# Kernel tuning notes

Measured on AMD Instinct MI355X. Metric: run time of the kernel, lower is better.

The kernel has to match this reference:

```python
import jax, jax.numpy as jnp
import numpy as np

B, T, I, H, L = 64, 2048, 128, 128, 2  # batch, seq_len, input, hidden, layers


def setup_inputs() -> dict:
    key = jax.random.key(0)
    ks = jax.random.split(key, 6)
    w = lambda k, shape: jax.random.normal(k, shape, dtype=jnp.float32) * 0.05
    return {
        "x": jax.random.normal(ks[0], (B, T, I), dtype=jnp.float32),
        "Wx0": w(ks[1], (4 * H, I)),
        "Wh0": w(ks[2], (4 * H, H)),
        "b0": jnp.zeros((4 * H,), jnp.float32),
        "Wx1": w(ks[3], (4 * H, H)),
        "Wh1": w(ks[4], (4 * H, H)),
        "b1": jnp.zeros((4 * H,), jnp.float32),
    }


def _cell(x_t, h, c, Wx, Wh, b):
    # fused-gate GEMM; gate order (i, f, g, o) matches the torch cell exactly
    gates = x_t @ Wx.T + h @ Wh.T + b  # [B, 4H]
    i, f, g, o = jnp.split(gates, 4, axis=-1)
    i = jax.nn.sigmoid(i)
    f = jax.nn.sigmoid(f)
    g = jnp.tanh(g)
    o = jax.nn.sigmoid(o)
    c_new = f * c + i * g
    h_new = o * jnp.tanh(c_new)
    return h_new, c_new


def reference(x, Wx0, Wh0, b0, Wx1, Wh1, b1):
    params = [(Wx0, Wh0, b0), (Wx1, Wh1, b1)]
    bsz = x.shape[0]
    hidden = Wh0.shape[1]
    h0 = jnp.zeros((L, bsz, hidden), x.dtype)
    c0 = jnp.zeros((L, bsz, hidden), x.dtype)

    def step(carry, x_t):
        h, c = carry
        hs, cs = [], []
        inp = x_t
        for l, (Wx, Wh, b) in enumerate(params):  # fixed, tiny layer loop
            hl, cl = _cell(inp, h[l], c[l], Wx, Wh, b)
            inp = hl
            hs.append(hl)
            cs.append(cl)
        return (jnp.stack(hs), jnp.stack(cs)), inp

    (hT, cT), ys = jax.lax.scan(step, (h0, c0), jnp.swapaxes(x, 0, 1))
    output = jnp.swapaxes(ys, 0, 1)  # [B, T, H], top-layer hidden states
    return output, hT, cT
```

## Files before the change

### kernel.cpp

```cpp
#include <hip/hip_runtime.h>
#include <hip/hip_fp16.h>

#define BB 64
#define TT 2048
#define II 128
#define HH 128
#define NG 512
#define CH 128
#define NCH (TT / CH)
#define DYN_LDS 81984

typedef _Float16 h2_t __attribute__((ext_vector_type(2)));

#if defined(__has_builtin)
#if __has_builtin(__builtin_amdgcn_fdot2)
#define HAVE_FDOT2 1
#endif
#endif

__device__ __forceinline__ float fdot2f(h2_t a, h2_t b, float c) {
#ifdef HAVE_FDOT2
  return __builtin_amdgcn_fdot2(a, b, c, false);
#else
  return c + (float)a[0] * (float)b[0] + (float)a[1] * (float)b[1];
#endif
}

__device__ __forceinline__ float fast_sigmoid(float x) {
  float t = __builtin_amdgcn_exp2f(-1.4426950408889634f * x);
  return __builtin_amdgcn_rcpf(1.0f + t);
}
__device__ __forceinline__ float act_gate(float x, bool tanh_sel) {
  float xx = tanh_sel ? 2.0f * x : x;
  float s = fast_sigmoid(xx);
  return tanh_sel ? 2.0f * s - 1.0f : s;
}
__device__ __forceinline__ float fast_tanh(float x) {
  return 2.0f * fast_sigmoid(2.0f * x) - 1.0f;
}

__device__ __forceinline__ float dpp_xor1(float x) {
  return __int_as_float(__builtin_amdgcn_update_dpp(0, __float_as_int(x), 0xB1, 0xF, 0xF, true));
}
__device__ __forceinline__ float dpp_xor2(float x) {
  return __int_as_float(__builtin_amdgcn_update_dpp(0, __float_as_int(x), 0x4E, 0xF, 0xF, true));
}

__device__ __forceinline__ void bar_lds() {
  __builtin_amdgcn_fence(__ATOMIC_RELEASE, "workgroup", "local");
  __builtin_amdgcn_s_barrier();
  __builtin_amdgcn_fence(__ATOMIC_ACQUIRE, "workgroup", "local");
}

union LD4 {
  float4 f4;
  h2_t h[4];
};
union LDB {
  uint4 u4;
  h2_t h[4];
};

__device__ __forceinline__ unsigned aload(unsigned* p) { return atomicAdd(p, 0u); }

__global__ void w_transpose2(const float* __restrict__ W0, float* __restrict__ T0,
                             const float* __restrict__ W1, float* __restrict__ T1) {
  int bid = blockIdx.x;
  const float* W = (bid < 256) ? W0 : W1;
  float* T = (bid < 256) ? T0 : T1;
  int idx = (bid & 255) * 256 + threadIdx.x;
  int n = idx >> 7;
  int k = idx & 127;
  T[k * NG + n] = W[idx];
}

__global__ __launch_bounds__(256) void xg_gemm_pro(const float* __restrict__ X,
                                                   const float* __restrict__ WT,
                                                   const float* __restrict__ bias,
                                                   __half* __restrict__ Xg) {
  __shared__ float As[64][132];
  __shared__ float Bs[128][64];
  const int bx = blockIdx.x;
  const size_t m0 = (size_t)(bx >> 2) * TT + (bx & 3) * 64;
  const int n0 = blockIdx.y * 64;
  const int tid = threadIdx.x;

  {
    const float4* xv = (const float4*)(X + m0 * II);
#pragma unroll
    for (int r = 0; r < 8; ++r) {
      int f = tid + 256 * r;
      int m = f >> 5;
      int c4 = f & 31;
      float4 v = xv[m * 32 + c4];
      *(float4*)&As[m][c4 * 4] = v;
    }
  }
  {
#pragma unroll
    for (int r = 0; r < 8; ++r) {
      int f = tid + 256 * r;
      int k = f >> 4;
      int q = f & 15;
      float4 v = *(const float4*)(WT + (size_t)k * NG + n0 + q * 4);
      *(float4*)&Bs[k][q * 4] = v;
    }
  }
  __syncthreads();

  const int tx = tid & 15;
  const int ty = tid >> 4;
  float acc[4][4];
#pragma unroll
  for (int i = 0; i < 4; ++i)
#pragma unroll
    for (int j = 0; j < 4; ++j) acc[i][j] = 0.0f;

#pragma unroll 4
  for (int k = 0; k < 128; ++k) {
    float a0 = As[ty * 4 + 0][k];
    float a1 = As[ty * 4 + 1][k];
    float a2 = As[ty * 4 + 2][k];
    float a3 = As[ty * 4 + 3][k];
    float4 bv = *(const float4*)&Bs[k][tx * 4];
    acc[0][0] = fmaf(a0, bv.x, acc[0][0]);
    acc[0][1] = fmaf(a0, bv.y, acc[0][1]);
    acc[0][2] = fmaf(a0, bv.z, acc[0][2]);
    acc[0][3] = fmaf(a0, bv.w, acc[0][3]);
    acc[1][0] = fmaf(a1, bv.x, acc[1][0]);
    acc[1][1] = fmaf(a1, bv.y, acc[1][1]);
    acc[1][2] = fmaf(a1, bv.z, acc[1][2]);
    acc[1][3] = fmaf(a1, bv.w, acc[1][3]);
    acc[2][0] = fmaf(a2, bv.x, acc[2][0]);
    acc[2][1] = fmaf(a2, bv.y, acc[2][1]);
    acc[2][2] = fmaf(a2, bv.z, acc[2][2]);
    acc[2][3] = fmaf(a2, bv.w, acc[2][3]);
    acc[3][0] = fmaf(a3, bv.x, acc[3][0]);
    acc[3][1] = fmaf(a3, bv.y, acc[3][1]);
    acc[3][2] = fmaf(a3, bv.z, acc[3][2]);
    acc[3][3] = fmaf(a3, bv.w, acc[3][3]);
  }

  float4 bvec = *(const float4*)(bias + n0 + tx * 4);
#pragma unroll
  for (int i = 0; i < 4; ++i) {
    size_t m = m0 + ty * 4 + i;
    __half2* dst = (__half2*)(Xg + m * NG + n0 + tx * 4);
    dst[0] = __halves2half2(__float2half(acc[i][0] + bvec.x),
                            __float2half(acc[i][1] + bvec.y));
    dst[1] = __halves2half2(__float2half(acc[i][2] + bvec.z),
                            __float2half(acc[i][3] + bvec.w));
  }
}


__device__ __forceinline__ void roleA(int b, int n, char* smem,
    const __half* Xg, const float* __restrict__ Wh0,
    float* __restrict__ out, __half* hstream,
    unsigned* flag0, unsigned* flagX)
{
  const int j = n >> 2;
  const int p = n & 3;
  const bool tsel = (p == 2);

  h2_t wh[4][16];
#pragma unroll
  for (int g = 0; g < 4; ++g) {
    const float2* ph = (const float2*)(Wh0 + (size_t)(g * 128 + j) * HH + p * 32);
#pragma unroll
    for (int k = 0; k < 16; ++k) {
      float2 v = ph[k];
      wh[g][k][0] = (_Float16)v.x;
      wh[g][k][1] = (_Float16)v.y;
    }
  }

  _Float16(*hb)[HH] = (_Float16(*)[HH])smem;
  if (n < HH) {
    hb[0][n] = (_Float16)0.0f;
    hb[1][n] = (_Float16)0.0f;
  }
  float c = 0.0f, hv = 0.0f;
  __syncthreads();

  const __half* xs = Xg + (size_t)b * TT * NG + p * 128 + j;
  float* hT = out + (size_t)BB * TT * HH;
  float* cT = hT + 2 * BB * HH;
  __half* hsp = hstream + (size_t)b * TT * HH + j;

#pragma unroll 1
  for (int cc = 0; cc < NCH; ++cc) {
    if (cc >= 2) {
      if (n == 0) {
        while (aload(flagX + b * NCH + cc) < 2u) __builtin_amdgcn_s_sleep(1);
      }
      __syncthreads();
      __builtin_amdgcn_fence(__ATOMIC_ACQUIRE, "agent");
    }
    __half xg_c = xs[(size_t)(cc * CH) * NG];

#pragma unroll 1
    for (int s = 0; s < CH; ++s) {
      const int i = cc * CH + s;
      __half xg_n = (s + 1 < CH) ? xs[(size_t)(i + 1) * NG] : __float2half(0.0f);

      const char* H = (const char*)hb[i & 1] + p * 64;
      float s0a = 0.f, s0b = 0.f, s1a = 0.f, s1b = 0.f;
      float s2a = 0.f, s2b = 0.f, s3a = 0.f, s3b = 0.f;
#pragma unroll
      for (int q = 0; q < 4; ++q) {
        LD4 u;
        u.f4 = *(const float4*)(H + q * 16);
        const int m = q * 4;
        s0a = fdot2f(wh[0][m + 0], u.h[0], s0a);
        s0b = fdot2f(wh[0][m + 2], u.h[2], s0b);
        s1a = fdot2f(wh[1][m + 0], u.h[0], s1a);
        s1b = fdot2f(wh[1][m + 2], u.h[2], s1b);
        s2a = fdot2f(wh[2][m + 0], u.h[0], s2a);
        s2b = fdot2f(wh[2][m + 2], u.h[2], s2b);
        s3a = fdot2f(wh[3][m + 0], u.h[0], s3a);
        s3b = fdot2f(wh[3][m + 2], u.h[2], s3b);
        s0a = fdot2f(wh[0][m + 1], u.h[1], s0a);
        s0b = fdot2f(wh[0][m + 3], u.h[3], s0b);
        s1a = fdot2f(wh[1][m + 1], u.h[1], s1a);
        s1b = fdot2f(wh[1][m + 3], u.h[3], s1b);
        s2a = fdot2f(wh[2][m + 1], u.h[1], s2a);
        s2b = fdot2f(wh[2][m + 3], u.h[3], s2b);
        s3a = fdot2f(wh[3][m + 1], u.h[1], s3a);
        s3b = fdot2f(wh[3][m + 3], u.h[3], s3b);
      }
      float a0 = s0a + s0b, a1 = s1a + s1b, a2 = s2a + s2b, a3 = s3a + s3b;

      float k01 = (p & 1) ? a1 : a0;
      float u01 = (p & 1) ? a0 : a1;
      float r01 = k01 + dpp_xor1(u01);
      float k23 = (p & 1) ? a3 : a2;
      float u23 = (p & 1) ? a2 : a3;
      float r23 = k23 + dpp_xor1(u23);
      float kA = (p & 2) ? r23 : r01;
      float uA = (p & 2) ? r01 : r23;
      float sL = kA + dpp_xor2(uA);
      float aL = act_gate(sL + __half2float(xg_c), tsel);
      float fg = dpp_xor1(aL);
      float gg = dpp_xor2(aL);
      float og = dpp_xor2(fg);
      if (p == 0) {
        c = fg * c + aL * gg;
        hv = og * fast_tanh(c);
        _Float16 hf = (_Float16)hv;
        hb[(i & 1) ^ 1][j] = hf;
        *(_Float16*)(hsp + (size_t)i * HH) = hf;
      }
      bar_lds();
      xg_c = xg_n;
    }
    __syncthreads();
    if (n == 0) {
      __builtin_amdgcn_fence(__ATOMIC_RELEASE, "agent");
      atomicExch(flag0 + b * NCH + cc, 1u);
    }
  }

  if (p == 0) {
    hT[b * HH + j] = hv;
    cT[b * HH + j] = c;
  }
}

__device__ __forceinline__ void roleC(int cidx, int n, char* smem,
    __half* Xg, const __half* hstream, const float* __restrict__ x,
    const float* __restrict__ WT0, const float* __restrict__ b0,
    const float* __restrict__ WT1, const float* __restrict__ b1,
    unsigned* flag0, unsigned* flagC, unsigned* flagX)
{
  const int b = cidx >> 1;
  const int half = cidx & 1;
  h2_t(*As2)[68] = (h2_t(*)[68])smem;
  h2_t(*Bs2)[64] = (h2_t(*)[64])(smem + 64 * 68 * 4);

  const int ty = n >> 4;
  const int tx = n & 15;
  const int mf = n >> 3;
  const int sf = n & 7;

#pragma unroll 1
  for (int cc = 0; cc < NCH; ++cc) {
    if (cc + 2 < NCH) {
      const int t0x = (cc + 2) * CH + half * 64;
      {
        const float4* sx = (const float4*)(x + ((size_t)b * TT + t0x + mf) * II + sf * 16);
        float4 p0 = sx[0], p1 = sx[1], p2 = sx[2], p3 = sx[3];
        h2_t r[8];
        r[0][0] = (_Float16)p0.x; r[0][1] = (_Float16)p0.y;
        r[1][0] = (_Float16)p0.z; r[1][1] = (_Float16)p0.w;
        r[2][0] = (_Float16)p1.x; r[2][1] = (_Float16)p1.y;
        r[3][0] = (_Float16)p1.z; r[3][1] = (_Float16)p1.w;
        r[4][0] = (_Float16)p2.x; r[4][1] = (_Float16)p2.y;
        r[5][0] = (_Float16)p2.z; r[5][1] = (_Float16)p2.w;
        r[6][0] = (_Float16)p3.x; r[6][1] = (_Float16)p3.y;
        r[7][0] = (_Float16)p3.z; r[7][1] = (_Float16)p3.w;
        *(uint4*)&As2[mf][sf * 8] = *(uint4*)&r[0];
        *(uint4*)&As2[mf][sf * 8 + 4] = *(uint4*)&r[4];
      }
#pragma unroll 1
      for (int nt = 0; nt < 8; ++nt) {
        __syncthreads();
        {
          const int kp = n >> 3, cg = n & 7;
          const float4* w0 = (const float4*)(WT0 + (size_t)(2 * kp) * NG + nt * 64 + cg * 8);
          const float4* w1 = (const float4*)(WT0 + (size_t)(2 * kp + 1) * NG + nt * 64 + cg * 8);
          float4 x0 = w0[0], x1 = w0[1];
          float4 y0 = w1[0], y1 = w1[1];
          h2_t r[8];
          r[0][0] = (_Float16)x0.x; r[0][1] = (_Float16)y0.x;
          r[1][0] = (_Float16)x0.y; r[1][1] = (_Float16)y0.y;
          r[2][0] = (_Float16)x0.z; r[2][1] = (_Float16)y0.z;
          r[3][0] = (_Float16)x0.w; r[3][1] = (_Float16)y0.w;
          r[4][0] = (_Float16)x1.x; r[4][1] = (_Float16)y1.x;
          r[5][0] = (_Float16)x1.y; r[5][1] = (_Float16)y1.y;
          r[6][0] = (_Float16)x1.z; r[6][1] = (_Float16)y1.z;
          r[7][0] = (_Float16)x1.w; r[7][1] = (_Float16)y1.w;
          *(uint4*)&Bs2[kp][cg * 8] = *(uint4*)&r[0];
          *(uint4*)&Bs2[kp][cg * 8 + 4] = *(uint4*)&r[4];
        }
        __syncthreads();

        float acc[2][4];
#pragma unroll
        for (int r = 0; r < 2; ++r)
#pragma unroll
          for (int q = 0; q < 4; ++q) acc[r][q] = 0.0f;
#pragma unroll 4
        for (int k4 = 0; k4 < 16; ++k4) {
          LDB ua0, ua1;
          ua0.u4 = *(const uint4*)&As2[ty * 2][k4 * 4];
          ua1.u4 = *(const uint4*)&As2[ty * 2 + 1][k4 * 4];
#pragma unroll
          for (int t = 0; t < 4; ++t) {
            LDB ub;
            ub.u4 = *(const uint4*)&Bs2[k4 * 4 + t][tx * 4];
            acc[0][0] = fdot2f(ua0.h[t], ub.h[0], acc[0][0]);
            acc[0][1] = fdot2f(ua0.h[t], ub.h[1], acc[0][1]);
            acc[0][2] = fdot2f(ua0.h[t], ub.h[2], acc[0][2]);
            acc[0][3] = fdot2f(ua0.h[t], ub.h[3], acc[0][3]);
            acc[1][0] = fdot2f(ua1.h[t], ub.h[0], acc[1][0]);
            acc[1][1] = fdot2f(ua1.h[t], ub.h[1], acc[1][1]);
            acc[1][2] = fdot2f(ua1.h[t], ub.h[2], acc[1][2]);
            acc[1][3] = fdot2f(ua1.h[t], ub.h[3], acc[1][3]);
          }
        }
        const int col = nt * 64 + tx * 4;
        float4 bv = *(const float4*)(b0 + col);
#pragma unroll
        for (int r = 0; r < 2; ++r) {
          __half2* d = (__half2*)(Xg + ((size_t)b * TT + t0x + ty * 2 + r) * NG + col);
          d[0] = __halves2half2(__float2half(acc[r][0] + bv.x),
                                __float2half(acc[r][1] + bv.y));
          d[1] = __halves2half2(__float2half(acc[r][2] + bv.z),
                                __float2half(acc[r][3] + bv.w));
        }
      }
      __syncthreads();
      if (n == 0) {
        __builtin_amdgcn_fence(__ATOMIC_RELEASE, "agent");
        atomicAdd(flagX + b * NCH + cc + 2, 1u);
      }
    }

    if (n == 0) {
      while (aload(flag0 + b * NCH + cc) < 1u) __builtin_amdgcn_s_sleep(8);
    }
    __syncthreads();
    __builtin_amdgcn_fence(__ATOMIC_ACQUIRE, "agent");

    const int t0 = cc * CH + half * 64;
    {
      const uint4* src = (const uint4*)(hstream + ((size_t)b * TT + t0 + mf) * HH + sf * 16);
      uint4 v0 = src[0], v1 = src[1];
      *(uint4*)&As2[mf][sf * 8] = v0;
      *(uint4*)&As2[mf][sf * 8 + 4] = v1;
    }
#pragma unroll 1
    for (int nt = 0; nt < 8; ++nt) {
      __syncthreads();
      {
        const int kp = n >> 3, cg = n & 7;
        const float4* w0 = (const float4*)(WT1 + (size_t)(2 * kp) * NG + nt * 64 + cg * 8);
        const float4* w1 = (const float4*)(WT1 + (size_t)(2 * kp + 1) * NG + nt * 64 + cg * 8);
        float4 x0 = w0[0], x1 = w0[1];
        float4 y0 = w1[0], y1 = w1[1];
        h2_t r[8];
        r[0][0] = (_Float16)x0.x; r[0][1] = (_Float16)y0.x;
        r[1][0] = (_Float16)x0.y; r[1][1] = (_Float16)y0.y;
        r[2][0] = (_Float16)x0.z; r[2][1] = (_Float16)y0.z;
        r[3][0] = (_Float16)x0.w; r[3][1] = (_Float16)y0.w;
        r[4][0] = (_Float16)x1.x; r[4][1] = (_Float16)y1.x;
        r[5][0] = (_Float16)x1.y; r[5][1] = (_Float16)y1.y;
        r[6][0] = (_Float16)x1.z; r[6][1] = (_Float16)y1.z;
        r[7][0] = (_Float16)x1.w; r[7][1] = (_Float16)y1.w;
        *(uint4*)&Bs2[kp][cg * 8] = *(uint4*)&r[0];
        *(uint4*)&Bs2[kp][cg * 8 + 4] = *(uint4*)&r[4];
      }
      __syncthreads();

      float acc[2][4];
#pragma unroll
      for (int r = 0; r < 2; ++r)
#pragma unroll
        for (int q = 0; q < 4; ++q) acc[r][q] = 0.0f;
#pragma unroll 4
      for (int k4 = 0; k4 < 16; ++k4) {
        LDB ua0, ua1;
        ua0.u4 = *(const uint4*)&As2[ty * 2][k4 * 4];
        ua1.u4 = *(const uint4*)&As2[ty * 2 + 1][k4 * 4];
#pragma unroll
        for (int t = 0; t < 4; ++t) {
          LDB ub;
          ub.u4 = *(const uint4*)&Bs2[k4 * 4 + t][tx * 4];
          acc[0][0] = fdot2f(ua0.h[t], ub.h[0], acc[0][0]);
          acc[0][1] = fdot2f(ua0.h[t], ub.h[1], acc[0][1]);
          acc[0][2] = fdot2f(ua0.h[t], ub.h[2], acc[0][2]);
          acc[0][3] = fdot2f(ua0.h[t], ub.h[3], acc[0][3]);
          acc[1][0] = fdot2f(ua1.h[t], ub.h[0], acc[1][0]);
          acc[1][1] = fdot2f(ua1.h[t], ub.h[1], acc[1][1]);
          acc[1][2] = fdot2f(ua1.h[t], ub.h[2], acc[1][2]);
          acc[1][3] = fdot2f(ua1.h[t], ub.h[3], acc[1][3]);
        }
      }
      const int col = nt * 64 + tx * 4;
      float4 bv = *(const float4*)(b1 + col);
#pragma unroll
      for (int r = 0; r < 2; ++r) {
        __half2* d = (__half2*)(Xg + ((size_t)b * TT + t0 + ty * 2 + r) * NG + col);
        d[0] = __halves2half2(__float2half(acc[r][0] + bv.x),
                              __float2half(acc[r][1] + bv.y));
        d[1] = __halves2half2(__float2half(acc[r][2] + bv.z),
                              __float2half(acc[r][3] + bv.w));
      }
    }
    __syncthreads();
    if (n == 0) {
      __builtin_amdgcn_fence(__ATOMIC_RELEASE, "agent");
      atomicAdd(flagC + b * NCH + cc, 1u);
    }
  }
}

__device__ __forceinline__ void roleB(int b, int n, char* smem,
    const __half* Xg, const float* __restrict__ Wh1,
    float* __restrict__ out, unsigned* flagC)
{
  const int j = n >> 2;
  const int p = n & 3;
  const bool tsel = (p == 2);

  h2_t wh[4][16];
#pragma unroll
  for (int g = 0; g < 4; ++g) {
    const float2* ph = (const float2*)(Wh1 + (size_t)(g * 128 + j) * HH + p * 32);
#pragma unroll
    for (int k = 0; k < 16; ++k) {
      float2 v = ph[k];
      wh[g][k][0] = (_Float16)v.x;
      wh[g][k][1] = (_Float16)v.y;
    }
  }

  _Float16(*hb)[HH] = (_Float16(*)[HH])smem;
  if (n < HH) {
    hb[0][n] = (_Float16)0.0f;
    hb[1][n] = (_Float16)0.0f;
  }
  float c = 0.0f, hv = 0.0f;
  __syncthreads();

  const __half* xs = Xg + (size_t)b * TT * NG + p * 128 + j;
  float* outp = out + (size_t)b * TT * HH;
  float* hT = out + (size_t)BB * TT * HH;
  float* cT = hT + 2 * BB * HH;

#pragma unroll 1
  for (int cc = 0; cc < NCH; ++cc) {
    if (n == 0) {
      while (aload(flagC + b * NCH + cc) < 2u) __builtin_amdgcn_s_sleep(8);
    }
    __syncthreads();
    __builtin_amdgcn_fence(__ATOMIC_ACQUIRE, "agent");

    __half xg_c = xs[(size_t)(cc * CH) * NG];
#pragma unroll 1
    for (int s = 0; s < CH; ++s) {
      const int i = cc * CH + s;
      __half xg_n = (s + 1 < CH) ? xs[(size_t)(i + 1) * NG] : __float2half(0.0f);

      const char* H = (const char*)hb[i & 1] + p * 64;
      float s0a = 0.f, s0b = 0.f, s1a = 0.f, s1b = 0.f;
      float s2a = 0.f, s2b = 0.f, s3a = 0.f, s3b = 0.f;
#pragma unroll
      for (int q = 0; q < 4; ++q) {
        LD4 u;
        u.f4 = *(const float4*)(H + q * 16);
        const int m = q * 4;
        s0a = fdot2f(wh[0][m + 0], u.h[0], s0a);
        s0b = fdot2f(wh[0][m + 2], u.h[2], s0b);
        s1a = fdot2f(wh[1][m + 0], u.h[0], s1a);
        s1b = fdot2f(wh[1][m + 2], u.h[2], s1b);
        s2a = fdot2f(wh[2][m + 0], u.h[0], s2a);
        s2b = fdot2f(wh[2][m + 2], u.h[2], s2b);
        s3a = fdot2f(wh[3][m + 0], u.h[0], s3a);
        s3b = fdot2f(wh[3][m + 2], u.h[2], s3b);
        s0a = fdot2f(wh[0][m + 1], u.h[1], s0a);
        s0b = fdot2f(wh[0][m + 3], u.h[3], s0b);
        s1a = fdot2f(wh[1][m + 1], u.h[1], s1a);
        s1b = fdot2f(wh[1][m + 3], u.h[3], s1b);
        s2a = fdot2f(wh[2][m + 1], u.h[1], s2a);
        s2b = fdot2f(wh[2][m + 3], u.h[3], s2b);
        s3a = fdot2f(wh[3][m + 1], u.h[1], s3a);
        s3b = fdot2f(wh[3][m + 3], u.h[3], s3b);
      }
      float a0 = s0a + s0b, a1 = s1a + s1b, a2 = s2a + s2b, a3 = s3a + s3b;

      float k01 = (p & 1) ? a1 : a0;
      float u01 = (p & 1) ? a0 : a1;
      float r01 = k01 + dpp_xor1(u01);
      float k23 = (p & 1) ? a3 : a2;
      float u23 = (p & 1) ? a2 : a3;
      float r23 = k23 + dpp_xor1(u23);
      float kA = (p & 2) ? r23 : r01;
      float uA = (p & 2) ? r01 : r23;
      float sL = kA + dpp_xor2(uA);
      float aL = act_gate(sL + __half2float(xg_c), tsel);
      float fg = dpp_xor1(aL);
      float gg = dpp_xor2(aL);
      float og = dpp_xor2(fg);
      if (p == 0) {
        c = fg * c + aL * gg;
        hv = og * fast_tanh(c);
        hb[(i & 1) ^ 1][j] = (_Float16)hv;
        outp[(size_t)i * HH + j] = hv;
      }
      bar_lds();
      xg_c = xg_n;
    }
  }

  if (p == 0) {
    hT[BB * HH + b * HH + j] = hv;
    cT[BB * HH + b * HH + j] = c;
  }
}

__global__
__attribute__((amdgpu_flat_work_group_size(512, 512)))
void lstm_mega(__half* Xg, __half* hstream, const float* __restrict__ x,
               const float* __restrict__ Wh0,
               const float* __restrict__ Wh1,
               const float* __restrict__ WT0,
               const float* __restrict__ b0,
               const float* __restrict__ WT1,
               const float* __restrict__ b1,
               float* __restrict__ out,
               unsigned* flag0, unsigned* flagC, unsigned* flagX)
{
  extern __shared__ __align__(16) char smem[];
  const int bid = blockIdx.x;
  const int n = threadIdx.x;
  if (bid < BB) {
    roleA(bid, n, smem, Xg, Wh0, out, hstream, flag0, flagX);
  } else if (bid < BB + 2 * BB) {
    roleC(bid - BB, n, smem, Xg, hstream, x, WT0, b0, WT1, b1,
          flag0, flagC, flagX);
  } else {
    roleB(bid - 3 * BB, n, smem, Xg, Wh1, out, flagC);
  }
}

extern "C" void kernel_launch(void* const* d_in, const int* in_sizes, int n_in,
                              void* d_out, int out_size, void* d_ws, size_t ws_size,
                              hipStream_t stream) {
  const float* x   = (const float*)d_in[0];
  const float* Wx0 = (const float*)d_in[1];
  const float* Wh0 = (const float*)d_in[2];
  const float* b0  = (const float*)d_in[3];
  const float* Wx1 = (const float*)d_in[4];
  const float* Wh1 = (const float*)d_in[5];
  const float* b1  = (const float*)d_in[6];
  float* out = (float*)d_out;

  char* base = (char*)d_ws;
  __half* Xg = (__half*)base;
  size_t off = (size_t)BB * TT * NG * sizeof(__half);
  __half* hstream = (__half*)(base + off);
  off += (size_t)BB * TT * HH * sizeof(__half);
  float* WT0 = (float*)(base + off);
  off += (size_t)II * NG * sizeof(float);
  float* WT1 = (float*)(base + off);
  off += (size_t)II * NG * sizeof(float);
  unsigned* flag0 = (unsigned*)(base + off);
  unsigned* flagC = flag0 + BB * NCH;
  unsigned* flagX = flagC + BB * NCH;

  static int attr_set = 0;
  hipFuncSetAttribute((const void*)lstm_mega,
                      hipFuncAttributeMaxDynamicSharedMemorySize, DYN_LDS);
  (void)attr_set;

  hipMemsetAsync(flag0, 0, 3 * (size_t)BB * NCH * sizeof(unsigned), stream);
  w_transpose2<<<512, 256, 0, stream>>>(Wx0, WT0, Wx1, WT1);
  xg_gemm_pro<<<dim3(BB * 4, NG / 64), 256, 0, stream>>>(x, WT0, b0, Xg);
  lstm_mega<<<4 * BB, 512, DYN_LDS, stream>>>(Xg, hstream, x, Wh0, Wh1, WT0,
                                              b0, WT1, b1, out, flag0, flagC,
                                              flagX);
}
```

Baseline: 1.415 ms.

## Deepen layer-0 input-projection prefetch lead and collapse dot-product accumulator chains

The prologue GEMM now precomputes the input projections for the first four chunks per batch instead of two, and the in-kernel producer role runs four chunks ahead of the recurrent consumer. This gives more slack between the helper GEMM and the serial recurrence, so the layer-0 loop should rarely wait on flagX. The recurrent dot products also go from two accumulators per gate to one, which shortens the reduction and frees registers but lengthens the dependent fdot2 chain. The larger prologue adds upfront latency before the megakernel starts.

Result: no change. 1.415 ms (median of 2 runs) (-0.0%).

```diff
diff --git a/kernel.cpp b/kernel.cpp
--- a/kernel.cpp
+++ b/kernel.cpp
@@ -8,6 +8,7 @@
 #define NG 512
 #define CH 128
 #define NCH (TT / CH)
+#define LEAD 4
 #define DYN_LDS 81984
 
 typedef _Float16 h2_t __attribute__((ext_vector_type(2)));
@@ -81,7 +82,7 @@
   __shared__ float As[64][132];
   __shared__ float Bs[128][64];
   const int bx = blockIdx.x;
-  const size_t m0 = (size_t)(bx >> 2) * TT + (bx & 3) * 64;
+  const size_t m0 = (size_t)(bx >> 3) * TT + (bx & 7) * 64;
   const int n0 = blockIdx.y * 64;
   const int tid = threadIdx.x;
 
@@ -190,7 +191,7 @@
 
 #pragma unroll 1
   for (int cc = 0; cc < NCH; ++cc) {
-    if (cc >= 2) {
+    if (cc >= LEAD) {
       if (n == 0) {
         while (aload(flagX + b * NCH + cc) < 2u) __builtin_amdgcn_s_sleep(1);
       }
@@ -205,31 +206,20 @@
       __half xg_n = (s + 1 < CH) ? xs[(size_t)(i + 1) * NG] : __float2half(0.0f);
 
       const char* H = (const char*)hb[i & 1] + p * 64;
-      float s0a = 0.f, s0b = 0.f, s1a = 0.f, s1b = 0.f;
-      float s2a = 0.f, s2b = 0.f, s3a = 0.f, s3b = 0.f;
+      float a0 = 0.f, a1 = 0.f, a2 = 0.f, a3 = 0.f;
 #pragma unroll
       for (int q = 0; q < 4; ++q) {
         LD4 u;
         u.f4 = *(const float4*)(H + q * 16);
-        const int m = q * 4;
-        s0a = fdot2f(wh[0][m + 0], u.h[0], s0a);
-        s0b = fdot2f(wh[0][m + 2], u.h[2], s0b);
-        s1a = fdot2f(wh[1][m + 0], u.h[0], s1a);
-        s1b = fdot2f(wh[1][m + 2], u.h[2], s1b);
-        s2a = fdot2f(wh[2][m + 0], u.h[0], s2a);
-        s2b = fdot2f(wh[2][m + 2], u.h[2], s2b);
-        s3a = fdot2f(wh[3][m + 0], u.h[0], s3a);
-        s3b = fdot2f(wh[3][m + 2], u.h[2], s3b);
-        s0a = fdot2f(wh[0][m + 1], u.h[1], s0a);
-        s0b = fdot2f(wh[0][m + 3], u.h[3], s0b);
-        s1a = fdot2f(wh[1][m + 1], u.h[1], s1a);
-        s1b = fdot2f(wh[1][m + 3], u.h[3], s1b);
-        s2a = fdot2f(wh[2][m + 1], u.h[1], s2a);
-        s2b = fdot2f(wh[2][m + 3], u.h[3], s2b);
-        s3a = fdot2f(wh[3][m + 1], u.h[1], s3a);
-        s3b = fdot2f(wh[3][m + 3], u.h[3], s3b);
-      }
-      float a0 = s0a + s0b, a1 = s1a + s1b, a2 = s2a + s2b, a3 = s3a + s3b;
+#pragma unroll
+        for (int t = 0; t < 4; ++t) {
+          const int m = q * 4 + t;
+          a0 = fdot2f(wh[0][m], u.h[t], a0);
+          a1 = fdot2f(wh[1][m], u.h[t], a1);
+          a2 = fdot2f(wh[2][m], u.h[t], a2);
+          a3 = fdot2f(wh[3][m], u.h[t], a3);
+        }
+      }
 
       float k01 = (p & 1) ? a1 : a0;
       float u01 = (p & 1) ? a0 : a1;
@@ -285,8 +275,8 @@
 
 #pragma unroll 1
   for (int cc = 0; cc < NCH; ++cc) {
-    if (cc + 2 < NCH) {
-      const int t0x = (cc + 2) * CH + half * 64;
+    if (cc + LEAD < NCH) {
+      const int t0x = (cc + LEAD) * CH + half * 64;
       {
         const float4* sx = (const float4*)(x + ((size_t)b * TT + t0x + mf) * II + sf * 16);
         float4 p0 = sx[0], p1 = sx[1], p2 = sx[2], p3 = sx[3];
@@ -363,7 +353,7 @@
       __syncthreads();
       if (n == 0) {
         __builtin_amdgcn_fence(__ATOMIC_RELEASE, "agent");
-        atomicAdd(flagX + b * NCH + cc + 2, 1u);
+        atomicAdd(flagX + b * NCH + cc + LEAD, 1u);
       }
     }
 
@@ -494,31 +484,20 @@
       __half xg_n = (s + 1 < CH) ? xs[(size_t)(i + 1) * NG] : __float2half(0.0f);
 
       const char* H = (const char*)hb[i & 1] + p * 64;
-      float s0a = 0.f, s0b = 0.f, s1a = 0.f, s1b = 0.f;
-      float s2a = 0.f, s2b = 0.f, s3a = 0.f, s3b = 0.f;
+      float a0 = 0.f, a1 = 0.f, a2 = 0.f, a3 = 0.f;
 #pragma unroll
       for (int q = 0; q < 4; ++q) {
         LD4 u;
         u.f4 = *(const float4*)(H + q * 16);
-        const int m = q * 4;
-        s0a = fdot2f(wh[0][m + 0], u.h[0], s0a);
-        s0b = fdot2f(wh[0][m + 2], u.h[2], s0b);
-        s1a = fdot2f(wh[1][m + 0], u.h[0], s1a);
-        s1b = fdot2f(wh[1][m + 2], u.h[2], s1b);
-        s2a = fdot2f(wh[2][m + 0], u.h[0], s2a);
-        s2b = fdot2f(wh[2][m + 2], u.h[2], s2b);
-        s3a = fdot2f(wh[3][m + 0], u.h[0], s3a);
-        s3b = fdot2f(wh[3][m + 2], u.h[2], s3b);
-        s0a = fdot2f(wh[0][m + 1], u.h[1], s0a);
-        s0b = fdot2f(wh[0][m + 3], u.h[3], s0b);
-        s1a = fdot2f(wh[1][m + 1], u.h[1], s1a);
-        s1b = fdot2f(wh[1][m + 3], u.h[3], s1b);
-        s2a = fdot2f(wh[2][m + 1], u.h[1], s2a);
-        s2b = fdot2f(wh[2][m + 3], u.h[3], s2b);
-        s3a = fdot2f(wh[3][m + 1], u.h[1], s3a);
-        s3b = fdot2f(wh[3][m + 3], u.h[3], s3b);
-      }
-      float a0 = s0a + s0b, a1 = s1a + s1b, a2 = s2a + s2b, a3 = s3a + s3b;
+#pragma unroll
+        for (int t = 0; t < 4; ++t) {
+          const int m = q * 4 + t;
+          a0 = fdot2f(wh[0][m], u.h[t], a0);
+          a1 = fdot2f(wh[1][m], u.h[t], a1);
+          a2 = fdot2f(wh[2][m], u.h[t], a2);
+          a3 = fdot2f(wh[3][m], u.h[t], a3);
+        }
+      }
 
       float k01 = (p & 1) ? a1 : a0;
       float u01 = (p & 1) ? a0 : a1;
@@ -600,14 +579,12 @@
   unsigned* flagC = flag0 + BB * NCH;
   unsigned* flagX = flagC + BB * NCH;
 
-  static int attr_set = 0;
   hipFuncSetAttribute((const void*)lstm_mega,
                       hipFuncAttributeMaxDynamicSharedMemorySize, DYN_LDS);
-  (void)attr_set;
 
   hipMemsetAsync(flag0, 0, 3 * (size_t)BB * NCH * sizeof(unsigned), stream);
   w_transpose2<<<512, 256, 0, stream>>>(Wx0, WT0, Wx1, WT1);
-  xg_gemm_pro<<<dim3(BB * 4, NG / 64), 256, 0, stream>>>(x, WT0, b0, Xg);
+  xg_gemm_pro<<<dim3(BB * 8, NG / 64), 256, 0, stream>>>(x, WT0, b0, Xg);
   lstm_mega<<<4 * BB, 512, DYN_LDS, stream>>>(Xg, hstream, x, Wh0, Wh1, WT0,
                                               b0, WT1, b1, out, flag0, flagC,
                                               flagX);
```
